# Kernel tuning notes

Measured on AMD Instinct MI355X. Metric: run time of the kernel, lower is better.

## Reference

```python
import jax, jax.numpy as jnp
import numpy as np

ZC, ZS = 32, 16
NS = [16384, 4096, 1024, 256, 64]  # mesh node counts per level
K_CH = 6
DEG = 12

def _key(i):
    return jax.random.fold_in(jax.random.key(0), i)

def setup_inputs():
    d = {}
    d["x"] = jax.random.normal(_key(0), (2, 16, NS[0], 3), jnp.float32)
    enc_dims = [(6, 16), (16, 16), (16, 16), (16, 32)]
    dec_dims = [(32, 16), (16, 16), (16, 16), (16, 3)]
    i = 1
    for p, dims in (("enc", enc_dims), ("decc", dec_dims), ("decs", dec_dims)):
        for l, (fi, fo) in enumerate(dims):
            d[p + "_W" + str(l)] = 0.1 * jax.random.normal(_key(i), (K_CH, fi, fo), jnp.float32); i += 1
            if p == "enc" or l < 3:  # last decoder convs have bias=None
                d[p + "_b" + str(l)] = jnp.zeros((fo,), jnp.float32)
    nfz = NS[4] * 32  # _n_features_before_z
    d["mu_W"] = 0.1 * jax.random.normal(_key(i), (ZC + ZS, nfz), jnp.float32); i += 1
    d["mu_b"] = jnp.zeros((ZC + ZS,), jnp.float32)
    d["linc_W"] = 0.1 * jax.random.normal(_key(i), (nfz, ZC), jnp.float32); i += 1
    d["linc_b"] = jnp.zeros((nfz,), jnp.float32)
    d["lins_W"] = 0.1 * jax.random.normal(_key(i), (nfz, ZC + 2 * ZS), jnp.float32); i += 1
    d["lins_b"] = jnp.zeros((nfz,), jnp.float32)
    for l in range(4):
        d["ei" + str(l)] = jax.random.randint(_key(i), (2, DEG * NS[l]), 0, NS[l], jnp.int32); i += 1
    d["ei4"] = jax.random.randint(_key(i), (2, DEG * NS[0]), 0, NS[0], jnp.int32); i += 1
    for l in range(4):
        d["ds_i" + str(l)] = jax.random.randint(_key(i), (NS[l + 1], 3), 0, NS[l], jnp.int32); i += 1
        d["ds_w" + str(l)] = jax.random.uniform(_key(i), (NS[l + 1], 3), jnp.float32); i += 1
        d["us_i" + str(l)] = jax.random.randint(_key(i), (NS[l], 3), 0, NS[l + 1], jnp.int32); i += 1
        d["us_w" + str(l)] = jax.random.uniform(_key(i), (NS[l], 3), jnp.float32); i += 1
    return d

def _norm(ei, n):
    # ChebConv_Coma.norm: D^-1/2 A D^-1/2 edge weights (unit edge weights)
    row, col = ei[0], ei[1]
    deg = jnp.zeros((n,), jnp.float32).at[row].add(1.0)
    dis = jnp.where(deg > 0, 1.0 / jnp.sqrt(jnp.maximum(deg, 1.0)), 0.0)
    return dis[row] * dis[col]

def _prop(x, ei, w, n):
    # sparse matvec: out[:, dst] += w_e * x[:, src]   (x: [B, n, F])
    msg = x[:, ei[0], :] * w[None, :, None]
    return jnp.zeros((x.shape[0], n, x.shape[2]), x.dtype).at[:, ei[1], :].add(msg)

def _cheb(x, ei, w, Wk, b, n):
    # Chebyshev recurrence: T0=x, T1=Lx, Tk=2L T_{k-1} - T_{k-2}
    out = jnp.einsum('bnf,fg->bng', x, Wk[0])
    Tx0 = x
    Tx1 = _prop(x, ei, w, n)
    out = out + jnp.einsum('bnf,fg->bng', Tx1, Wk[1])
    for k in range(2, Wk.shape[0]):
        Tx2 = 2.0 * _prop(Tx1, ei, w, n) - Tx0
        out = out + jnp.einsum('bnf,fg->bng', Tx2, Wk[k])
        Tx0, Tx1 = Tx1, Tx2
    return out if b is None else out + b

def _pool(x, idx, w):
    # sparse pooling matrix, 3 nnz/row: out[:, i] = sum_k w[i,k] * x[:, idx[i,k]]
    return jnp.einsum('bnkf,nk->bnf', x[:, idx, :], w)

def _phase(x):
    # PhaseTensor: doubles last dim with cos/sin phase modulation over time axis 1
    T = x.shape[1]
    th = 2.0 * jnp.pi * jnp.arange(T, dtype=x.dtype) / T
    shp = (1, T) + (1,) * (x.ndim - 2)
    return jnp.concatenate([x * jnp.cos(th).reshape(shp), x * jnp.sin(th).reshape(shp)], axis=-1)

def _model(FL, IL):
    (x, eW0, eb0, eW1, eb1, eW2, eb2, eW3, eb3,
     cW0, cb0, cW1, cb1, cW2, cb2, cW3,
     sW0, sb0, sW1, sb1, sW2, sb2, sW3,
     mu_W, mu_b, linc_W, linc_b, lins_W, lins_b,
     ds_w0, ds_w1, ds_w2, ds_w3, us_w0, us_w1, us_w2, us_w3) = FL
    (ei0, ei1, ei2, ei3, ei4,
     ds_i0, ds_i1, ds_i2, ds_i3, us_i0, us_i1, us_i2, us_i3) = IL
    eis = [ei0, ei1, ei2, ei3, ei4]
    lvl_n = [NS[0], NS[1], NS[2], NS[3], NS[0]]
    nrm = [_norm(eis[l], lvl_n[l]) for l in range(5)]
    B, T, N0, F0 = x.shape
    # phase_input: [B,T,N,3] -> [B,T,N,6]; fold time into batch for the conv stack
    h = _phase(x).reshape(B * T, N0, 2 * F0)
    encW = [(eW0, eb0), (eW1, eb1), (eW2, eb2), (eW3, eb3)]
    dsl = [(ds_i0, ds_w0), (ds_i1, ds_w1), (ds_i2, ds_w2), (ds_i3, ds_w3)]
    usl = [(us_i0, us_w0), (us_i1, us_w1), (us_i2, us_w2), (us_i3, us_w3)]
    for l in range(4):
        h = jax.nn.relu(_cheb(h, eis[l], nrm[l], encW[l][0], encW[l][1], NS[l]))
        h = _pool(h, dsl[l][0], dsl[l][1])
    h = h.reshape(B, T, -1)  # [B, T, N4*32]
    mu = jnp.einsum('btf,zf->btz', h, mu_W) + mu_b
    # faithful to torch code: per-t cat along dim 0 (time-major) then reshape(-1, T, z)
    mu_c = jnp.mean(jnp.swapaxes(mu[..., :ZC], 0, 1).reshape(B, T, ZC), axis=1)
    mu_s = jnp.mean(jnp.swapaxes(mu[..., ZC:], 0, 1).reshape(B, T, ZS), axis=1)

    def dec(z, Ws, bs, lW, lb, relu_first):
        y = z @ lW.T + lb
        if relu_first:
            y = jax.nn.relu(y)
        y = y.reshape(y.shape[0], NS[4], Ws[0].shape[1])  # [*, N4, 32]
        for i in range(3):  # n_layers - 1 upsample+conv+relu
            lvl = 3 - i
            y = _pool(y, usl[lvl][0], usl[lvl][1])
            y = jax.nn.relu(_cheb(y, eis[lvl], nrm[lvl], Ws[i], bs[i], NS[lvl]))
        y = _pool(y, usl[0][0], usl[0][1])
        return _cheb(y, eis[4], nrm[4], Ws[3], None, NS[0])  # final conv, no bias/relu

    s_avg = dec(mu_c, [cW0, cW1, cW2, cW3], [cb0, cb1, cb2], linc_W, linc_b, False)
    # decoder_s, vectorized over timeframes by folding T into batch
    zs_ph = _phase(jnp.broadcast_to(mu_s[:, None, :], (B, T, ZS)))  # [B,T,2*ZS]
    zc_rep = jnp.broadcast_to(mu_c[:, None, :], (B, T, ZC))
    zin = jnp.concatenate([zc_rep, zs_ph], axis=-1).reshape(B * T, ZC + 2 * ZS)
    ds_t = dec(zin, [sW0, sW1, sW2, sW3], [sb0, sb1, sb2], lins_W, lins_b, True).reshape(B, T, N0, 3)
    s_t = s_avg[:, None] + ds_t
    return mu_c, mu_s, s_avg, s_t

def reference(x, enc_W0, enc_b0, enc_W1, enc_b1, enc_W2, enc_b2, enc_W3, enc_b3, decc_W0, decc_b0, decc_W1, decc_b1, decc_W2, decc_b2, decc_W3, decs_W0, decs_b0, decs_W1, decs_b1, decs_W2, decs_b2, decs_W3, mu_W, mu_b, linc_W, linc_b, lins_W, lins_b, ds_w0, ds_w1, ds_w2, ds_w3, us_w0, us_w1, us_w2, us_w3, ei0, ei1, ei2, ei3, ei4, ds_i0, ds_i1, ds_i2, ds_i3, us_i0, us_i1, us_i2, us_i3):
    FL = (x, enc_W0, enc_b0, enc_W1, enc_b1, enc_W2, enc_b2, enc_W3, enc_b3,
          decc_W0, decc_b0, decc_W1, decc_b1, decc_W2, decc_b2, decc_W3,
          decs_W0, decs_b0, decs_W1, decs_b1, decs_W2, decs_b2, decs_W3,
          mu_W, mu_b, linc_W, linc_b, lins_W, lins_b,
          ds_w0, ds_w1, ds_w2, ds_w3, us_w0, us_w1, us_w2, us_w3)
    IL = (ei0, ei1, ei2, ei3, ei4, ds_i0, ds_i1, ds_i2, ds_i3, us_i0, us_i1, us_i2, us_i3)
    return _model(FL, IL)
```

## Files before the change

### kernel.cpp

```cpp
#include <hip/hip_runtime.h>
#include <cstdint>
#include <cstddef>

#define TPB 256

typedef float f32x4 __attribute__((ext_vector_type(4)));
typedef float f32x2 __attribute__((ext_vector_type(2)));
typedef int   i32x4 __attribute__((ext_vector_type(4)));

static inline int cdiv(long long a, int b){ return (int)((a + (long long)b - 1) / b); }

#define NTOT 38144
#define ETOT 457728
#define CTOT 762880
#define RPTOT 38149


template<int W>
__device__ __forceinline__ void vload(const float* __restrict__ p, float* r){
  if constexpr (W == 8){ vload<4>(p, r); vload<4>(p+4, r+4); }
  else if constexpr (W == 4){ f32x4 v = *reinterpret_cast<const f32x4*>(p); r[0]=v.x;r[1]=v.y;r[2]=v.z;r[3]=v.w; }
  else { f32x2 v = *reinterpret_cast<const f32x2*>(p); r[0]=v.x;r[1]=v.y; }
}
template<int W>
__device__ __forceinline__ void vstore(float* __restrict__ p, const float* r){
  if constexpr (W == 8){ vstore<4>(p, r); vstore<4>(p+4, r+4); }
  else if constexpr (W == 4){ f32x4 v; v.x=r[0];v.y=r[1];v.z=r[2];v.w=r[3]; *reinterpret_cast<f32x4*>(p) = v; }
  else { f32x2 v; v.x=r[0];v.y=r[1]; *reinterpret_cast<f32x2*>(p) = v; }
}

template<int F>
__device__ __forceinline__ void loadrow(const float* __restrict__ p, float* r){
  #pragma unroll
  for (int q = 0; q < F/4; ++q) vload<4>(p + 4*q, r + 4*q);
}
template<int F>
__device__ __forceinline__ void storerow(float* __restrict__ p, const float* r){
  #pragma unroll
  for (int q = 0; q < F/4; ++q) vstore<4>(p + 4*q, r + 4*q);
}


__device__ __forceinline__ bool lvl_edge(int t, const int* e0,const int* e1,const int* e2,const int* e3,const int* e4,
                                         const int*& ei, int& E, int& noff, int& rpoff, int& rel){
  if (t < 196608){ ei=e0; E=196608; noff=0;     rpoff=0;     rel=t;        return true; }
  if (t < 245760){ ei=e1; E=49152;  noff=16384; rpoff=16385; rel=t-196608; return true; }
  if (t < 258048){ ei=e2; E=12288;  noff=20480; rpoff=20482; rel=t-245760; return true; }
  if (t < 261120){ ei=e3; E=3072;   noff=21504; rpoff=21507; rel=t-258048; return true; }
  if (t < 457728){ ei=e4; E=196608; noff=21760; rpoff=21764; rel=t-261120; return true; }
  return false;
}

__global__ void k_degs_all(const int* e0,const int* e1,const int* e2,const int* e3,const int* e4,
                           int* __restrict__ rowdeg, int* __restrict__ dstdeg){
  int t = blockIdx.x*blockDim.x + threadIdx.x;
  const int* ei; int E, noff, rpoff, rel;
  if (!lvl_edge(t, e0,e1,e2,e3,e4, ei,E,noff,rpoff,rel)) return;
  atomicAdd(&rowdeg[noff + ei[rel]], 1);
  atomicAdd(&dstdeg[noff + ei[E + rel]], 1);
}

__global__ void k_dis_all(const int* __restrict__ rowdeg, float* __restrict__ dis){
  int t = blockIdx.x*blockDim.x + threadIdx.x;
  if (t >= NTOT) return;
  int d = rowdeg[t];
  dis[t] = d > 0 ? rsqrtf((float)d) : 0.f;
}

__global__ void k_scan5(const int* __restrict__ dstdeg, int* __restrict__ rp, int* __restrict__ cursor){
  const int NnA[5]  = {16384,4096,1024,256,16384};
  const int NOFF[5] = {0,16384,20480,21504,21760};
  const int COFF[5] = {0,327680,409600,430080,435200};
  __shared__ int part[257];
  int l = blockIdx.x;
  int N = NnA[l];
  const int* cnt = dstdeg + NOFF[l];
  int* rpl = rp + NOFF[l] + l;
  int* cul = cursor + NOFF[l] + l;
  int tid = threadIdx.x;
  int chunk = (N + 255) / 256;
  int lo = tid*chunk; if (lo > N) lo = N;
  int hi = lo + chunk; if (hi > N) hi = N;
  int s = 0;
  for (int i = lo; i < hi; ++i) s += (cnt[i] + 7) & ~7;
  part[tid+1] = s;
  if (tid == 0) part[0] = COFF[l];
  __syncthreads();
  if (tid == 0){ for (int i = 1; i <= 256; ++i) part[i] += part[i-1]; }
  __syncthreads();
  int run = part[tid];
  for (int i = lo; i < hi; ++i){ rpl[i] = run; cul[i] = run; run += (cnt[i] + 7) & ~7; }
  if (tid == 0) rpl[N] = part[256];
}

__global__ void k_fill_all(const int* e0,const int* e1,const int* e2,const int* e3,const int* e4,
                           const float* __restrict__ dis, int* __restrict__ cursor,
                           int* __restrict__ srcs, float* __restrict__ w){
  int t = blockIdx.x*blockDim.x + threadIdx.x;
  const int* ei; int E, noff, rpoff, rel;
  if (!lvl_edge(t, e0,e1,e2,e3,e4, ei,E,noff,rpoff,rel)) return;
  int src = ei[rel], dst = ei[E + rel];
  int pos = atomicAdd(&cursor[rpoff + dst], 1);
  srcs[pos] = src;
  w[pos] = dis[noff + src] * dis[noff + dst];
}

__global__ void k_pad_all(const int* __restrict__ dstdeg, const int* __restrict__ rp,
                          int* __restrict__ srcs, float* __restrict__ w){
  int t = blockIdx.x*blockDim.x + threadIdx.x;
  if (t >= NTOT) return;
  int rpoff, n;
  if      (t < 16384){ rpoff = 0;     n = t; }
  else if (t < 20480){ rpoff = 16385; n = t - 16384; }
  else if (t < 21504){ rpoff = 20482; n = t - 20480; }
  else if (t < 21760){ rpoff = 21507; n = t - 21504; }
  else               { rpoff = 21764; n = t - 21760; }
  int j0 = rp[rpoff + n];
  int j1 = rp[rpoff + n + 1];
  int cnt = dstdeg[t];
  int sfill = cnt > 0 ? srcs[j0] : 0;
  for (int j = j0 + cnt; j < j1; ++j){ srcs[j] = sfill; w[j] = 0.f; }
}


template<int FPL, int FinPad>
__device__ __forceinline__ void gather8(const float* __restrict__ gb,
                                        const int* __restrict__ srcs, const float* __restrict__ w,
                                        int j0, int j1, int sub, float* acc){
  #pragma unroll
  for (int q = 0; q < FPL; ++q) acc[q] = 0.f;
  for (int j = j0; j < j1; j += 8){
    i32x4 sa = *reinterpret_cast<const i32x4*>(srcs + j);
    i32x4 sb = *reinterpret_cast<const i32x4*>(srcs + j + 4);
    f32x4 wa = *reinterpret_cast<const f32x4*>(w + j);
    f32x4 wb = *reinterpret_cast<const f32x4*>(w + j + 4);
    float v0[FPL], v1[FPL], v2[FPL], v3[FPL], v4[FPL], v5[FPL], v6[FPL], v7[FPL];
    vload<FPL>(gb + (size_t)sa.x*FinPad + sub*FPL, v0);
    vload<FPL>(gb + (size_t)sa.y*FinPad + sub*FPL, v1);
    vload<FPL>(gb + (size_t)sa.z*FinPad + sub*FPL, v2);
    vload<FPL>(gb + (size_t)sa.w*FinPad + sub*FPL, v3);
    vload<FPL>(gb + (size_t)sb.x*FinPad + sub*FPL, v4);
    vload<FPL>(gb + (size_t)sb.y*FinPad + sub*FPL, v5);
    vload<FPL>(gb + (size_t)sb.z*FinPad + sub*FPL, v6);
    vload<FPL>(gb + (size_t)sb.w*FinPad + sub*FPL, v7);
    #pragma unroll
    for (int q = 0; q < FPL; ++q){
      acc[q] = fmaf(wa.x, v0[q], acc[q]);
      acc[q] = fmaf(wa.y, v1[q], acc[q]);
      acc[q] = fmaf(wa.z, v2[q], acc[q]);
      acc[q] = fmaf(wa.w, v3[q], acc[q]);
      acc[q] = fmaf(wb.x, v4[q], acc[q]);
      acc[q] = fmaf(wb.y, v5[q], acc[q]);
      acc[q] = fmaf(wb.z, v6[q], acc[q]);
      acc[q] = fmaf(wb.w, v7[q], acc[q]);
    }
  }
}

template<int FinPad, int FinReal, int Fout>
__device__ __forceinline__ void gemm_acc(const float* ts, const float* __restrict__ Wk,
                                         int sub, int lanebase, float* o){
  constexpr int FPL = FinPad/4;
  float tv[FinPad];
  #pragma unroll
  for (int s = 0; s < 4; ++s)
    #pragma unroll
    for (int q = 0; q < FPL; ++q)
      tv[s*FPL+q] = __shfl(ts[q], lanebase + s, 64);
  if constexpr (Fout % 4 == 0){
    constexpr int OPL = Fout/4;
    #pragma unroll
    for (int fi = 0; fi < FinReal; ++fi)
      #pragma unroll
      for (int q = 0; q < OPL; ++q)
        o[q] = fmaf(tv[fi], Wk[fi*Fout + sub*OPL + q], o[q]);
  } else {
    if (sub < Fout){
      #pragma unroll
      for (int fi = 0; fi < FinReal; ++fi)
        o[0] = fmaf(tv[fi], Wk[fi*Fout + sub], o[0]);
    }
  }
}

__device__ __forceinline__ long long swz_i(int G){
  int bid = blockIdx.x, nb = gridDim.x;
  if (G == 32 && (nb & 31) == 0){
    int bpg = nb >> 5;
    int xcd = bid & 7, j = bid >> 3;
    int gi = j / bpg, nc = j - gi*bpg;
    bid = ((gi << 3) | xcd) * bpg + nc;
  }
  return (long long)bid * blockDim.x + threadIdx.x;
}

template<int FinPad, int PRE>
__device__ __forceinline__ void pre_row(const float* __restrict__ psrc, const int* __restrict__ pidx,
                                        const float* __restrict__ pw, int n, int g, int Nin, int sub,
                                        float* r){
  constexpr int FPL = FinPad/4;
  if constexpr (PRE == 1){
    int t = g & 15;
    float th = 6.283185307179586f * (float)t / 16.0f;
    float sn, cs; sincosf(th, &sn, &cs);
    const float* xr = psrc + ((size_t)g*16384 + n)*3;
    #pragma unroll
    for (int q = 0; q < FPL; ++q){
      int c = sub*FPL + q;
      float v = 0.f;
      if (c < 6) v = xr[c % 3] * (c < 3 ? cs : sn);
      r[q] = v;
    }
  } else {
    int i0 = pidx[n*3+0], i1 = pidx[n*3+1], i2 = pidx[n*3+2];
    float w0 = pw[n*3+0], w1 = pw[n*3+1], w2 = pw[n*3+2];
    const float* bsrc = psrc + (size_t)g*Nin*FinPad + sub*FPL;
    float a[FPL], b[FPL], c[FPL];
    vload<FPL>(bsrc + (size_t)i0*FinPad, a);
    vload<FPL>(bsrc + (size_t)i1*FinPad, b);
    vload<FPL>(bsrc + (size_t)i2*FinPad, c);
    #pragma unroll
    for (int q = 0; q < FPL; ++q) r[q] = fmaf(w0, a[q], fmaf(w1, b[q], w2*c[q]));
  }
}


template<int FinPad, int PRE>
__global__ void k_pre_f(const float* __restrict__ psrc, const int* __restrict__ pidx,
                        const float* __restrict__ pw, float* __restrict__ bufX,
                        int G, int logN, int Nin){
  constexpr int FPL = FinPad/4;
  long long i4 = swz_i(G);
  if (i4 >= ((long long)G << logN)*4) return;
  int sub = (int)(i4 & 3);
  long long i = i4 >> 2;
  int N = 1 << logN;
  int n = (int)(i & (N-1));
  int g = (int)(i >> logN);
  float r[FPL];
  pre_row<FinPad,PRE>(psrc, pidx, pw, n, g, Nin, sub, r);
  vstore<FPL>(bufX + (size_t)i*FinPad + sub*FPL, r);
}

template<int FinPad, int FinReal, int Fout>
__global__ void k_first_f(const int* __restrict__ rp, const int* __restrict__ srcs, const float* __restrict__ w,
                          const float* __restrict__ bufX, float* __restrict__ bufT1, float* __restrict__ out,
                          const float* __restrict__ W6, const float* __restrict__ bias,
                          int G, int logN){
  constexpr int FPL = FinPad/4;
  constexpr int OPL = (Fout % 4 == 0) ? Fout/4 : 1;
  long long i4 = swz_i(G);
  if (i4 >= ((long long)G << logN)*4) return;
  int sub = (int)(i4 & 3);
  long long i = i4 >> 2;
  int N = 1 << logN;
  int n = (int)(i & (N-1));
  int lanebase = ((int)threadIdx.x & 63) & ~3;
  const float* gb = bufX + (size_t)(i - n)*FinPad;
  float t0[FPL]; vload<FPL>(bufX + (size_t)i*FinPad + sub*FPL, t0);
  float t1[FPL];
  gather8<FPL,FinPad>(gb, srcs, w, rp[n], rp[n+1], sub, t1);
  vstore<FPL>(bufT1 + (size_t)i*FinPad + sub*FPL, t1);
  float o[OPL];
  if constexpr (Fout % 4 == 0){
    #pragma unroll
    for (int q = 0; q < OPL; ++q) o[q] = bias ? bias[sub*OPL + q] : 0.f;
  } else {
    o[0] = (bias && sub < Fout) ? bias[sub] : 0.f;
  }
  gemm_acc<FinPad,FinReal,Fout>(t0, W6, sub, lanebase, o);
  gemm_acc<FinPad,FinReal,Fout>(t1, W6 + (size_t)FinReal*Fout, sub, lanebase, o);
  if constexpr (Fout % 4 == 0) vstore<OPL>(out + (size_t)i*Fout + sub*OPL, o);
  else if (sub < Fout) out[(size_t)i*Fout + sub] = o[0];
}

template<int FinPad, int FinReal, int Fout>
__global__ void k_step_f(const int* __restrict__ rp, const int* __restrict__ srcs, const float* __restrict__ w,
                         const float* __restrict__ Tm1, float* __restrict__ P, float* __restrict__ out,
                         const float* __restrict__ Wk, const float* __restrict__ savg,
                         int G, int logN, int relu, int last){
  constexpr int FPL = FinPad/4;
  constexpr int OPL = (Fout % 4 == 0) ? Fout/4 : 1;
  long long i4 = swz_i(G);
  if (i4 >= ((long long)G << logN)*4) return;
  int sub = (int)(i4 & 3);
  long long i = i4 >> 2;
  int N = 1 << logN;
  int n = (int)(i & (N-1));
  int lanebase = ((int)threadIdx.x & 63) & ~3;
  const float* gb = Tm1 + (size_t)(i - n)*FinPad;
  float tk[FPL];
  gather8<FPL,FinPad>(gb, srcs, w, rp[n], rp[n+1], sub, tk);
  float tm2[FPL]; vload<FPL>(P + (size_t)i*FinPad + sub*FPL, tm2);
  #pragma unroll
  for (int q = 0; q < FPL; ++q) tk[q] = 2.f*tk[q] - tm2[q];
  if (!last) vstore<FPL>(P + (size_t)i*FinPad + sub*FPL, tk);
  float o[OPL];
  if constexpr (Fout % 4 == 0) vload<OPL>(out + (size_t)i*Fout + sub*OPL, o);
  else { o[0] = (sub < Fout) ? out[(size_t)i*Fout + sub] : 0.f; }
  gemm_acc<FinPad,FinReal,Fout>(tk, Wk, sub, lanebase, o);
  if constexpr (Fout % 4 == 0){
    if (last && relu){
      #pragma unroll
      for (int q = 0; q < OPL; ++q) o[q] = fmaxf(o[q], 0.f);
    }
    vstore<OPL>(out + (size_t)i*Fout + sub*OPL, o);
  } else {
    if (sub < Fout){
      float v = o[0];
      if (last && relu) v = fmaxf(v, 0.f);
      if (last && savg){
        int g = (int)(i >> logN);
        int b = g >> 4;
        v += savg[((size_t)b*N + n)*3 + sub];
      }
      out[(size_t)i*Fout + sub] = v;
    }
  }
}


template<int F>
__global__ void k_pool_t(const float* __restrict__ X, const int* __restrict__ idx,
                         const float* __restrict__ w, float* __restrict__ out,
                         int G, int Nin, int Nout){
  long long i = (long long)blockIdx.x*blockDim.x + threadIdx.x;
  if (i >= (long long)G*Nout) return;
  int n = (int)(i % Nout), g = (int)(i / Nout);
  int i0 = idx[n*3+0], i1 = idx[n*3+1], i2 = idx[n*3+2];
  float w0 = w[n*3+0], w1 = w[n*3+1], w2 = w[n*3+2];
  const float* b = X + (size_t)g*Nin*F;
  float r0[F], r1[F], r2[F], o[F];
  loadrow<F>(b + (size_t)i0*F, r0);
  loadrow<F>(b + (size_t)i1*F, r1);
  loadrow<F>(b + (size_t)i2*F, r2);
  #pragma unroll
  for (int f = 0; f < F; ++f)
    o[f] = fmaf(w0, r0[f], fmaf(w1, r1[f], w2 * r2[f]));
  storerow<F>(out + ((size_t)g*Nout + n)*F, o);
}

__global__ void k_mu(const float* __restrict__ h, const float* __restrict__ W,
                     const float* __restrict__ b, float* __restrict__ mu){
  int wid = (blockIdx.x*blockDim.x + threadIdx.x) >> 6;
  int lane = threadIdx.x & 63;
  if (wid >= 32*48) return;
  int z = wid % 48, g = wid / 48;
  const float* hr = h + (size_t)g*2048;
  const float* wr = W + (size_t)z*2048;
  float acc = 0.f;
  for (int f = lane; f < 2048; f += 64) acc = fmaf(hr[f], wr[f], acc);
  for (int o = 32; o > 0; o >>= 1) acc += __shfl_down(acc, o, 64);
  if (lane == 0) mu[wid] = acc + b[z];
}

__global__ void k_mucs(const float* __restrict__ mu, float* __restrict__ muc,
                       float* __restrict__ mus, float* __restrict__ out){
  int i = blockIdx.x*blockDim.x + threadIdx.x;
  if (i >= 96) return;
  int z = i % 48, bp = i / 48;
  float acc = 0.f;
  for (int b = 0; b < 2; ++b)
    for (int t = 8*bp; t < 8*bp + 8; ++t)
      acc += mu[(b*16 + t)*48 + z];
  acc *= (1.f/16.f);
  if (z < 32){ muc[bp*32 + z] = acc; out[bp*32 + z] = acc; }
  else       { mus[bp*16 + (z-32)] = acc; out[64 + bp*16 + (z-32)] = acc; }
}

__global__ void k_zin(const float* __restrict__ muc, const float* __restrict__ mus,
                      float* __restrict__ zin){
  int i = blockIdx.x*blockDim.x + threadIdx.x;
  if (i >= 32*64) return;
  int c = i % 64, g = i / 64;
  int b = g / 16, t = g % 16;
  float v;
  if (c < 32){
    v = muc[b*32 + c];
  } else {
    float th = 6.283185307179586f * (float)t / 16.0f;
    int k = c - 32;
    int kk = (k < 16) ? k : (k - 16);
    float m = mus[b*16 + kk];
    v = (k < 16) ? m * cosf(th) : m * sinf(th);
  }
  zin[i] = v;
}

__global__ void k_lin(const float* __restrict__ z, const float* __restrict__ W,
                      const float* __restrict__ b, float* __restrict__ y,
                      int G, int Z, int relu){
  int i = blockIdx.x*blockDim.x + threadIdx.x;
  if (i >= G*2048) return;
  int f = i % 2048, g = i / 2048;
  const float* zr = z + (size_t)g*Z;
  const float* wr = W + (size_t)f*Z;
  float acc = b[f];
  for (int k = 0; k < Z; ++k) acc = fmaf(zr[k], wr[k], acc);
  if (relu) acc = fmaxf(acc, 0.f);
  y[i] = acc;
}


struct LvlArgs {
  const int* rp; const int* srcs; const float* w;
  const float* psrc; const int* pidx; const float* pw;
  float* bufX; float* bufT1; float* out;
  const float* W6; const float* bias; const float* savg;
  int G; int logN; int Nin; int relu;
};

template<int FinPad, int FinReal, int Fout, int PRE>
static void run_level(hipStream_t s, const LvlArgs& a){
  long long GN4 = ((long long)a.G << a.logN) * 4;
  int grid = cdiv(GN4, 256);
  k_pre_f<FinPad,PRE><<<grid,256,0,s>>>(a.psrc, a.pidx, a.pw, a.bufX, a.G, a.logN, a.Nin);
  k_first_f<FinPad,FinReal,Fout><<<grid,256,0,s>>>(a.rp, a.srcs, a.w, a.bufX, a.bufT1, a.out,
                                                   a.W6, a.bias, a.G, a.logN);
  float* Ab = a.bufT1; float* Bb = a.bufX;
  for (int k = 2; k <= 5; ++k){
    int last = (k == 5) ? 1 : 0;
    k_step_f<FinPad,FinReal,Fout><<<grid,256,0,s>>>(a.rp, a.srcs, a.w, Ab, Bb, a.out,
                                                    a.W6 + (size_t)k*FinReal*Fout,
                                                    last ? a.savg : nullptr,
                                                    a.G, a.logN, a.relu, last);
    float* t = Ab; Ab = Bb; Bb = t;
  }
}

extern "C" void kernel_launch(void* const* d_in, const int* in_sizes, int n_in,
                              void* d_out, int out_size, void* d_ws, size_t ws_size,
                              hipStream_t stream){
  const float* x = (const float*)d_in[0];
  const float* encW[4] = {(const float*)d_in[1],(const float*)d_in[3],(const float*)d_in[5],(const float*)d_in[7]};
  const float* encB[4] = {(const float*)d_in[2],(const float*)d_in[4],(const float*)d_in[6],(const float*)d_in[8]};
  const float* ccW[4]  = {(const float*)d_in[9],(const float*)d_in[11],(const float*)d_in[13],(const float*)d_in[15]};
  const float* ccB[3]  = {(const float*)d_in[10],(const float*)d_in[12],(const float*)d_in[14]};
  const float* csW[4]  = {(const float*)d_in[16],(const float*)d_in[18],(const float*)d_in[20],(const float*)d_in[22]};
  const float* csB[3]  = {(const float*)d_in[17],(const float*)d_in[19],(const float*)d_in[21]};
  const float* muW  = (const float*)d_in[23]; const float* muB  = (const float*)d_in[24];
  const float* lincW = (const float*)d_in[25]; const float* lincB = (const float*)d_in[26];
  const float* linsW = (const float*)d_in[27]; const float* linsB = (const float*)d_in[28];
  const int* ei[5] = {(const int*)d_in[29],(const int*)d_in[30],(const int*)d_in[31],
                      (const int*)d_in[32],(const int*)d_in[33]};
  const int* ds_i[4]; const float* ds_w[4]; const int* us_i[4]; const float* us_w[4];
  for (int l = 0; l < 4; ++l){
    ds_i[l] = (const int*)d_in[34 + 4*l]; ds_w[l] = (const float*)d_in[35 + 4*l];
    us_i[l] = (const int*)d_in[36 + 4*l]; us_w[l] = (const float*)d_in[37 + 4*l];
  }

  float* ws = (float*)d_ws;
  const size_t BIG = 8388608;
  float* B0 = ws + 0*BIG;
  float* B1 = ws + 1*BIG;
  float* B2 = ws + 2*BIG;
  float* B3 = ws + 3*BIG;
  size_t off = 4*BIG;

  int*   rp_all     = (int*)(ws + off); off += RPTOT;
  int*   cursor_all = (int*)(ws + off); off += RPTOT;
  off = (off + 3) & ~(size_t)3;
  int*   srcs_all   = (int*)(ws + off); off += CTOT;
  float* w_all      =        ws + off;  off += CTOT;
  int*   rowdeg     = (int*)(ws + off); off += NTOT;
  int*   dstdeg     = (int*)(ws + off); off += NTOT;
  float* dis        =        ws + off;  off += NTOT;
  float* hmu        =        ws + off;  off += (size_t)32*2048;
  float* mu         =        ws + off;  off += (size_t)32*48;
  float* muc        =        ws + off;  off += 64;
  float* mus        =        ws + off;  off += 32;
  float* zin        =        ws + off;  off += (size_t)32*64;

  float* outp = (float*)d_out;
  float* out_savg = outp + 96;
  float* out_st   = outp + 96 + 98304;

  hipMemsetAsync(rowdeg, 0, 2*(size_t)NTOT*sizeof(int), stream);
  k_degs_all<<<cdiv(ETOT,TPB),TPB,0,stream>>>(ei[0],ei[1],ei[2],ei[3],ei[4], rowdeg, dstdeg);
  k_dis_all<<<cdiv(NTOT,TPB),TPB,0,stream>>>(rowdeg, dis);
  k_scan5<<<5,256,0,stream>>>(dstdeg, rp_all, cursor_all);
  k_fill_all<<<cdiv(ETOT,TPB),TPB,0,stream>>>(ei[0],ei[1],ei[2],ei[3],ei[4], dis, cursor_all, srcs_all, w_all);
  k_pad_all<<<cdiv(NTOT,TPB),TPB,0,stream>>>(dstdeg, rp_all, srcs_all, w_all);

  const int RPOFF[5] = {0,16385,20482,21507,21764};
  const int* RP[5];
  for (int l = 0; l < 5; ++l) RP[l] = rp_all + RPOFF[l];

  run_level<8,6,16,1>(stream, {RP[0],srcs_all,w_all, x,nullptr,nullptr,
                               B0,B1,B2, encW[0],encB[0],nullptr, 32,14,0,1});
  run_level<16,16,16,0>(stream, {RP[1],srcs_all,w_all, B2,ds_i[0],ds_w[0],
                                 B0,B1,B3, encW[1],encB[1],nullptr, 32,12,16384,1});
  run_level<16,16,16,0>(stream, {RP[2],srcs_all,w_all, B3,ds_i[1],ds_w[1],
                                 B0,B1,B2, encW[2],encB[2],nullptr, 32,10,4096,1});
  run_level<16,16,32,0>(stream, {RP[3],srcs_all,w_all, B2,ds_i[2],ds_w[2],
                                 B0,B1,B3, encW[3],encB[3],nullptr, 32,8,1024,1});
  k_pool_t<32><<<cdiv((long long)32*64,TPB),TPB,0,stream>>>(B3, ds_i[3], ds_w[3], hmu, 32, 256, 64);

  k_mu<<<cdiv((long long)32*48*64,TPB),TPB,0,stream>>>(hmu, muW, muB, mu);
  k_mucs<<<1,128,0,stream>>>(mu, muc, mus, outp);

  k_lin<<<cdiv((long long)2*2048,TPB),TPB,0,stream>>>(muc, lincW, lincB, B2, 2, 32, 0);
  run_level<32,32,16,0>(stream, {RP[3],srcs_all,w_all, B2,us_i[3],us_w[3],
                                 B0,B1,B3, ccW[0],ccB[0],nullptr, 2,8,64,1});
  run_level<16,16,16,0>(stream, {RP[2],srcs_all,w_all, B3,us_i[2],us_w[2],
                                 B0,B1,B2, ccW[1],ccB[1],nullptr, 2,10,256,1});
  run_level<16,16,16,0>(stream, {RP[1],srcs_all,w_all, B2,us_i[1],us_w[1],
                                 B0,B1,B3, ccW[2],ccB[2],nullptr, 2,12,1024,1});
  run_level<16,16,3,0>(stream, {RP[4],srcs_all,w_all, B3,us_i[0],us_w[0],
                                B0,B1,out_savg, ccW[3],nullptr,nullptr, 2,14,4096,0});

  k_zin<<<cdiv(32*64,TPB),TPB,0,stream>>>(muc, mus, zin);
  k_lin<<<cdiv((long long)32*2048,TPB),TPB,0,stream>>>(zin, linsW, linsB, B2, 32, 64, 1);
  run_level<32,32,16,0>(stream, {RP[3],srcs_all,w_all, B2,us_i[3],us_w[3],
                                 B0,B1,B3, csW[0],csB[0],nullptr, 32,8,64,1});
  run_level<16,16,16,0>(stream, {RP[2],srcs_all,w_all, B3,us_i[2],us_w[2],
                                 B0,B1,B2, csW[1],csB[1],nullptr, 32,10,256,1});
  run_level<16,16,16,0>(stream, {RP[1],srcs_all,w_all, B2,us_i[1],us_w[1],
                                 B0,B1,B3, csW[2],csB[2],nullptr, 32,12,1024,1});
  run_level<16,16,3,0>(stream, {RP[4],srcs_all,w_all, B3,us_i[0],us_w[0],
                                B0,B1,out_st, csW[3],nullptr,out_savg, 32,14,4096,0});

  (void)in_sizes; (void)n_in; (void)out_size; (void)ws_size;
}
```

Before: 1.326 ms.

## Interleave four graphs per node row for batched Chebyshev convolutions

Adds a transposed layout for the 32-graph paths: each node row now holds the features of four graphs side by side, and the grid is split into eight graph-groups with one group per block-index residue mod 8. Each gathered neighbour index then serves four graphs with one contiguous fetch, which cuts index and weight loads and improves the coalescing of the sparse gather. The pooling, mu projection and lins linear kernels are rewritten to produce or consume this layout. The 2-graph content decoder keeps the old layout without the XCD swizzle. The cost is more complex indexing and wider per-row footprints.

```diff
diff --git a/kernel.cpp b/kernel.cpp
--- a/kernel.cpp
+++ b/kernel.cpp
@@ -123,6 +123,192 @@
 }
 
 
+template<int FinPad>
+__device__ __forceinline__ void tmap(int N, int& gb, int& n, int& gs, int& sub, int& laneoff){
+  constexpr int LPR = FinPad/4;
+  gb = blockIdx.x & 7;
+  int I = (blockIdx.x >> 3)*256 + threadIdx.x;
+  n = I / FinPad;
+  int u = I - n*FinPad;
+  gs = u / LPR;
+  sub = u - gs*LPR;
+  laneoff = gs*FinPad + sub*4;
+}
+
+template<int FinPad>
+__device__ __forceinline__ void gather8_t(const float* __restrict__ base,
+                                          const int* __restrict__ srcs, const float* __restrict__ w,
+                                          int j0, int j1, int laneoff, float* acc){
+  constexpr int RS = 4*FinPad;
+  #pragma unroll
+  for (int q = 0; q < 4; ++q) acc[q] = 0.f;
+  for (int j = j0; j < j1; j += 8){
+    i32x4 sa = *reinterpret_cast<const i32x4*>(srcs + j);
+    i32x4 sb = *reinterpret_cast<const i32x4*>(srcs + j + 4);
+    f32x4 wa = *reinterpret_cast<const f32x4*>(w + j);
+    f32x4 wb = *reinterpret_cast<const f32x4*>(w + j + 4);
+    float v0[4], v1[4], v2[4], v3[4], v4[4], v5[4], v6[4], v7[4];
+    vload<4>(base + (size_t)sa.x*RS + laneoff, v0);
+    vload<4>(base + (size_t)sa.y*RS + laneoff, v1);
+    vload<4>(base + (size_t)sa.z*RS + laneoff, v2);
+    vload<4>(base + (size_t)sa.w*RS + laneoff, v3);
+    vload<4>(base + (size_t)sb.x*RS + laneoff, v4);
+    vload<4>(base + (size_t)sb.y*RS + laneoff, v5);
+    vload<4>(base + (size_t)sb.z*RS + laneoff, v6);
+    vload<4>(base + (size_t)sb.w*RS + laneoff, v7);
+    #pragma unroll
+    for (int q = 0; q < 4; ++q){
+      acc[q] = fmaf(wa.x, v0[q], acc[q]);
+      acc[q] = fmaf(wa.y, v1[q], acc[q]);
+      acc[q] = fmaf(wa.z, v2[q], acc[q]);
+      acc[q] = fmaf(wa.w, v3[q], acc[q]);
+      acc[q] = fmaf(wb.x, v4[q], acc[q]);
+      acc[q] = fmaf(wb.y, v5[q], acc[q]);
+      acc[q] = fmaf(wb.z, v6[q], acc[q]);
+      acc[q] = fmaf(wb.w, v7[q], acc[q]);
+    }
+  }
+}
+
+template<int FinPad, int FinReal, int Fout>
+__device__ __forceinline__ void gemm_t(const float* ts, const float* __restrict__ Wk,
+                                       int sub, float* o){
+  constexpr int LPR = FinPad/4;
+  int lane = (int)threadIdx.x & 63;
+  int lanebase = lane & ~(LPR-1);
+  float tv[FinPad];
+  #pragma unroll
+  for (int s = 0; s < LPR; ++s)
+    #pragma unroll
+    for (int q = 0; q < 4; ++q)
+      tv[s*4+q] = __shfl(ts[q], lanebase + s, 64);
+  if constexpr (Fout % 4 == 0){
+    constexpr int OPL = Fout/LPR;
+    #pragma unroll
+    for (int fi = 0; fi < FinReal; ++fi)
+      #pragma unroll
+      for (int q = 0; q < OPL; ++q)
+        o[q] = fmaf(tv[fi], Wk[fi*Fout + sub*OPL + q], o[q]);
+  } else {
+    if (sub < Fout){
+      #pragma unroll
+      for (int fi = 0; fi < FinReal; ++fi)
+        o[0] = fmaf(tv[fi], Wk[fi*Fout + sub], o[0]);
+    }
+  }
+}
+
+template<int FinPad, int PRE>
+__global__ void k_pre_t(const float* __restrict__ psrc, const int* __restrict__ pidx,
+                        const float* __restrict__ pw, float* __restrict__ bufX,
+                        int N, int Nin){
+  int gb, n, gs, sub, laneoff;
+  tmap<FinPad>(N, gb, n, gs, sub, laneoff);
+  constexpr int RS = 4*FinPad;
+  float r[4];
+  if constexpr (PRE == 1){
+    int g = (gb<<2) | gs;
+    int t = g & 15;
+    float th = 6.283185307179586f * (float)t / 16.0f;
+    float sn, cs; sincosf(th, &sn, &cs);
+    const float* xr = psrc + ((size_t)g*16384 + n)*3;
+    #pragma unroll
+    for (int q = 0; q < 4; ++q){
+      int f = sub*4 + q;
+      float v = 0.f;
+      if (f < 6) v = xr[f % 3] * (f < 3 ? cs : sn);
+      r[q] = v;
+    }
+  } else {
+    int i0 = pidx[n*3+0], i1 = pidx[n*3+1], i2 = pidx[n*3+2];
+    float w0 = pw[n*3+0], w1 = pw[n*3+1], w2 = pw[n*3+2];
+    const float* pb = psrc + (size_t)gb*Nin*RS + laneoff;
+    float a[4], b[4], c[4];
+    vload<4>(pb + (size_t)i0*RS, a);
+    vload<4>(pb + (size_t)i1*RS, b);
+    vload<4>(pb + (size_t)i2*RS, c);
+    #pragma unroll
+    for (int q = 0; q < 4; ++q) r[q] = fmaf(w0, a[q], fmaf(w1, b[q], w2*c[q]));
+  }
+  vstore<4>(bufX + (size_t)gb*N*RS + (size_t)n*RS + laneoff, r);
+}
+
+template<int FinPad, int FinReal, int Fout>
+__global__ void k_first_t(const int* __restrict__ rp, const int* __restrict__ srcs, const float* __restrict__ w,
+                          const float* __restrict__ bufX, float* __restrict__ bufT1, float* __restrict__ out,
+                          const float* __restrict__ W6, const float* __restrict__ bias, int N){
+  constexpr int LPR = FinPad/4;
+  constexpr int OPL = (Fout % 4 == 0) ? Fout/LPR : 1;
+  constexpr int RS = 4*FinPad;
+  int gb, n, gs, sub, laneoff;
+  tmap<FinPad>(N, gb, n, gs, sub, laneoff);
+  const float* gbase = bufX + (size_t)gb*N*RS;
+  float t0[4]; vload<4>(gbase + (size_t)n*RS + laneoff, t0);
+  float t1[4];
+  gather8_t<FinPad>(gbase, srcs, w, rp[n], rp[n+1], laneoff, t1);
+  vstore<4>(bufT1 + (size_t)gb*N*RS + (size_t)n*RS + laneoff, t1);
+  float o[OPL];
+  if constexpr (Fout % 4 == 0){
+    #pragma unroll
+    for (int q = 0; q < OPL; ++q) o[q] = bias ? bias[sub*OPL + q] : 0.f;
+  } else {
+    o[0] = (bias && sub < Fout) ? bias[sub] : 0.f;
+  }
+  gemm_t<FinPad,FinReal,Fout>(t0, W6, sub, o);
+  gemm_t<FinPad,FinReal,Fout>(t1, W6 + (size_t)FinReal*Fout, sub, o);
+  if constexpr (Fout % 4 == 0){
+    vstore<OPL>(out + ((size_t)(gb*N + n)*4 + gs)*Fout + sub*OPL, o);
+  } else {
+    if (sub < Fout){
+      int g = (gb<<2)|gs;
+      out[((size_t)g*N + n)*3 + sub] = o[0];
+    }
+  }
+}
+
+template<int FinPad, int FinReal, int Fout>
+__global__ void k_step_t(const int* __restrict__ rp, const int* __restrict__ srcs, const float* __restrict__ w,
+                         const float* __restrict__ Tm1, float* __restrict__ P, float* __restrict__ out,
+                         const float* __restrict__ Wk, const float* __restrict__ savg,
+                         int N, int relu, int last){
+  constexpr int LPR = FinPad/4;
+  constexpr int OPL = (Fout % 4 == 0) ? Fout/LPR : 1;
+  constexpr int RS = 4*FinPad;
+  int gb, n, gs, sub, laneoff;
+  tmap<FinPad>(N, gb, n, gs, sub, laneoff);
+  const float* gbase = Tm1 + (size_t)gb*N*RS;
+  float tk[4];
+  gather8_t<FinPad>(gbase, srcs, w, rp[n], rp[n+1], laneoff, tk);
+  float tm2[4]; vload<4>(P + (size_t)gb*N*RS + (size_t)n*RS + laneoff, tm2);
+  #pragma unroll
+  for (int q = 0; q < 4; ++q) tk[q] = 2.f*tk[q] - tm2[q];
+  if (!last) vstore<4>(P + (size_t)gb*N*RS + (size_t)n*RS + laneoff, tk);
+  float o[OPL];
+  if constexpr (Fout % 4 == 0){
+    vload<OPL>(out + ((size_t)(gb*N + n)*4 + gs)*Fout + sub*OPL, o);
+  } else {
+    o[0] = 0.f;
+    if (sub < Fout) o[0] = out[((size_t)((gb<<2)|gs)*N + n)*3 + sub];
+  }
+  gemm_t<FinPad,FinReal,Fout>(tk, Wk, sub, o);
+  if constexpr (Fout % 4 == 0){
+    if (last && relu){
+      #pragma unroll
+      for (int q = 0; q < OPL; ++q) o[q] = fmaxf(o[q], 0.f);
+    }
+    vstore<OPL>(out + ((size_t)(gb*N + n)*4 + gs)*Fout + sub*OPL, o);
+  } else {
+    if (sub < Fout){
+      float v = o[0];
+      if (last && relu) v = fmaxf(v, 0.f);
+      int g = (gb<<2)|gs;
+      if (last && savg) v += savg[((size_t)(g>>4)*N + n)*3 + sub];
+      out[((size_t)g*N + n)*3 + sub] = v;
+    }
+  }
+}
+
+
 template<int FPL, int FinPad>
 __device__ __forceinline__ void gather8(const float* __restrict__ gb,
                                         const int* __restrict__ srcs, const float* __restrict__ w,
@@ -183,54 +369,28 @@
   }
 }
 
-__device__ __forceinline__ long long swz_i(int G){
-  int bid = blockIdx.x, nb = gridDim.x;
-  if (G == 32 && (nb & 31) == 0){
-    int bpg = nb >> 5;
-    int xcd = bid & 7, j = bid >> 3;
-    int gi = j / bpg, nc = j - gi*bpg;
-    bid = ((gi << 3) | xcd) * bpg + nc;
-  }
-  return (long long)bid * blockDim.x + threadIdx.x;
-}
-
-template<int FinPad, int PRE>
-__device__ __forceinline__ void pre_row(const float* __restrict__ psrc, const int* __restrict__ pidx,
-                                        const float* __restrict__ pw, int n, int g, int Nin, int sub,
-                                        float* r){
+template<int FinPad>
+__device__ __forceinline__ void pool_row(const float* __restrict__ psrc, const int* __restrict__ pidx,
+                                         const float* __restrict__ pw, int n, int g, int Nin, int sub,
+                                         float* r){
   constexpr int FPL = FinPad/4;
-  if constexpr (PRE == 1){
-    int t = g & 15;
-    float th = 6.283185307179586f * (float)t / 16.0f;
-    float sn, cs; sincosf(th, &sn, &cs);
-    const float* xr = psrc + ((size_t)g*16384 + n)*3;
-    #pragma unroll
-    for (int q = 0; q < FPL; ++q){
-      int c = sub*FPL + q;
-      float v = 0.f;
-      if (c < 6) v = xr[c % 3] * (c < 3 ? cs : sn);
-      r[q] = v;
-    }
-  } else {
-    int i0 = pidx[n*3+0], i1 = pidx[n*3+1], i2 = pidx[n*3+2];
-    float w0 = pw[n*3+0], w1 = pw[n*3+1], w2 = pw[n*3+2];
-    const float* bsrc = psrc + (size_t)g*Nin*FinPad + sub*FPL;
-    float a[FPL], b[FPL], c[FPL];
-    vload<FPL>(bsrc + (size_t)i0*FinPad, a);
-    vload<FPL>(bsrc + (size_t)i1*FinPad, b);
-    vload<FPL>(bsrc + (size_t)i2*FinPad, c);
-    #pragma unroll
-    for (int q = 0; q < FPL; ++q) r[q] = fmaf(w0, a[q], fmaf(w1, b[q], w2*c[q]));
-  }
-}
-
-
-template<int FinPad, int PRE>
+  int i0 = pidx[n*3+0], i1 = pidx[n*3+1], i2 = pidx[n*3+2];
+  float w0 = pw[n*3+0], w1 = pw[n*3+1], w2 = pw[n*3+2];
+  const float* bsrc = psrc + (size_t)g*Nin*FinPad + sub*FPL;
+  float a[FPL], b[FPL], c[FPL];
+  vload<FPL>(bsrc + (size_t)i0*FinPad, a);
+  vload<FPL>(bsrc + (size_t)i1*FinPad, b);
+  vload<FPL>(bsrc + (size_t)i2*FinPad, c);
+  #pragma unroll
+  for (int q = 0; q < FPL; ++q) r[q] = fmaf(w0, a[q], fmaf(w1, b[q], w2*c[q]));
+}
+
+template<int FinPad>
 __global__ void k_pre_f(const float* __restrict__ psrc, const int* __restrict__ pidx,
                         const float* __restrict__ pw, float* __restrict__ bufX,
                         int G, int logN, int Nin){
   constexpr int FPL = FinPad/4;
-  long long i4 = swz_i(G);
+  long long i4 = (long long)blockIdx.x*blockDim.x + threadIdx.x;
   if (i4 >= ((long long)G << logN)*4) return;
   int sub = (int)(i4 & 3);
   long long i = i4 >> 2;
@@ -238,7 +398,7 @@
   int n = (int)(i & (N-1));
   int g = (int)(i >> logN);
   float r[FPL];
-  pre_row<FinPad,PRE>(psrc, pidx, pw, n, g, Nin, sub, r);
+  pool_row<FinPad>(psrc, pidx, pw, n, g, Nin, sub, r);
   vstore<FPL>(bufX + (size_t)i*FinPad + sub*FPL, r);
 }
 
@@ -249,7 +409,7 @@
                           int G, int logN){
   constexpr int FPL = FinPad/4;
   constexpr int OPL = (Fout % 4 == 0) ? Fout/4 : 1;
-  long long i4 = swz_i(G);
+  long long i4 = (long long)blockIdx.x*blockDim.x + threadIdx.x;
   if (i4 >= ((long long)G << logN)*4) return;
   int sub = (int)(i4 & 3);
   long long i = i4 >> 2;
@@ -281,7 +441,7 @@
                          int G, int logN, int relu, int last){
   constexpr int FPL = FinPad/4;
   constexpr int OPL = (Fout % 4 == 0) ? Fout/4 : 1;
-  long long i4 = swz_i(G);
+  long long i4 = (long long)blockIdx.x*blockDim.x + threadIdx.x;
   if (i4 >= ((long long)G << logN)*4) return;
   int sub = (int)(i4 & 3);
   long long i = i4 >> 2;
@@ -311,8 +471,7 @@
       if (last && relu) v = fmaxf(v, 0.f);
       if (last && savg){
         int g = (int)(i >> logN);
-        int b = g >> 4;
-        v += savg[((size_t)b*N + n)*3 + sub];
+        v += savg[((size_t)(g>>4)*N + n)*3 + sub];
       }
       out[(size_t)i*Fout + sub] = v;
     }
@@ -320,36 +479,17 @@
 }
 
 
-template<int F>
-__global__ void k_pool_t(const float* __restrict__ X, const int* __restrict__ idx,
-                         const float* __restrict__ w, float* __restrict__ out,
-                         int G, int Nin, int Nout){
-  long long i = (long long)blockIdx.x*blockDim.x + threadIdx.x;
-  if (i >= (long long)G*Nout) return;
-  int n = (int)(i % Nout), g = (int)(i / Nout);
-  int i0 = idx[n*3+0], i1 = idx[n*3+1], i2 = idx[n*3+2];
-  float w0 = w[n*3+0], w1 = w[n*3+1], w2 = w[n*3+2];
-  const float* b = X + (size_t)g*Nin*F;
-  float r0[F], r1[F], r2[F], o[F];
-  loadrow<F>(b + (size_t)i0*F, r0);
-  loadrow<F>(b + (size_t)i1*F, r1);
-  loadrow<F>(b + (size_t)i2*F, r2);
-  #pragma unroll
-  for (int f = 0; f < F; ++f)
-    o[f] = fmaf(w0, r0[f], fmaf(w1, r1[f], w2 * r2[f]));
-  storerow<F>(out + ((size_t)g*Nout + n)*F, o);
-}
-
-__global__ void k_mu(const float* __restrict__ h, const float* __restrict__ W,
-                     const float* __restrict__ b, float* __restrict__ mu){
+__global__ void k_mu_t(const float* __restrict__ h_t, const float* __restrict__ W,
+                       const float* __restrict__ b, float* __restrict__ mu){
   int wid = (blockIdx.x*blockDim.x + threadIdx.x) >> 6;
   int lane = threadIdx.x & 63;
   if (wid >= 32*48) return;
   int z = wid % 48, g = wid / 48;
-  const float* hr = h + (size_t)g*2048;
   const float* wr = W + (size_t)z*2048;
+  const float* hb = h_t + (size_t)(g>>2)*64*128 + (g&3)*32;
   float acc = 0.f;
-  for (int f = lane; f < 2048; f += 64) acc = fmaf(hr[f], wr[f], acc);
+  for (int f2 = lane; f2 < 2048; f2 += 64)
+    acc = fmaf(hb[(size_t)(f2>>5)*128 + (f2&31)], wr[f2], acc);
   for (int o = 32; o > 0; o >>= 1) acc += __shfl_down(acc, o, 64);
   if (lane == 0) mu[wid] = acc + b[z];
 }
@@ -401,6 +541,20 @@
   y[i] = acc;
 }
 
+__global__ void k_lin_t(const float* __restrict__ z, const float* __restrict__ W,
+                        const float* __restrict__ b, float* __restrict__ y_t,
+                        int Z, int relu){
+  int i = blockIdx.x*blockDim.x + threadIdx.x;
+  if (i >= 32*2048) return;
+  int f2 = i % 2048, g = i / 2048;
+  const float* zr = z + (size_t)g*Z;
+  const float* wr = W + (size_t)f2*Z;
+  float acc = b[f2];
+  for (int k = 0; k < Z; ++k) acc = fmaf(zr[k], wr[k], acc);
+  if (relu) acc = fmaxf(acc, 0.f);
+  y_t[(size_t)(g>>2)*64*128 + (size_t)(f2>>5)*128 + (g&3)*32 + (f2&31)] = acc;
+}
+
 
 struct LvlArgs {
   const int* rp; const int* srcs; const float* w;
@@ -411,10 +565,28 @@
 };
 
 template<int FinPad, int FinReal, int Fout, int PRE>
-static void run_level(hipStream_t s, const LvlArgs& a){
+static void run_level_t(hipStream_t s, const LvlArgs& a){
+  int N = 1 << a.logN;
+  int grid = 8 * (N*FinPad/256);
+  k_pre_t<FinPad,PRE><<<grid,256,0,s>>>(a.psrc, a.pidx, a.pw, a.bufX, N, a.Nin);
+  k_first_t<FinPad,FinReal,Fout><<<grid,256,0,s>>>(a.rp, a.srcs, a.w, a.bufX, a.bufT1, a.out,
+                                                   a.W6, a.bias, N);
+  float* Ab = a.bufT1; float* Bb = a.bufX;
+  for (int k = 2; k <= 5; ++k){
+    int last = (k == 5) ? 1 : 0;
+    k_step_t<FinPad,FinReal,Fout><<<grid,256,0,s>>>(a.rp, a.srcs, a.w, Ab, Bb, a.out,
+                                                    a.W6 + (size_t)k*FinReal*Fout,
+                                                    last ? a.savg : nullptr,
+                                                    N, a.relu, last);
+    float* t = Ab; Ab = Bb; Bb = t;
+  }
+}
+
+template<int FinPad, int FinReal, int Fout>
+static void run_level_f(hipStream_t s, const LvlArgs& a){
   long long GN4 = ((long long)a.G << a.logN) * 4;
   int grid = cdiv(GN4, 256);
-  k_pre_f<FinPad,PRE><<<grid,256,0,s>>>(a.psrc, a.pidx, a.pw, a.bufX, a.G, a.logN, a.Nin);
+  k_pre_f<FinPad><<<grid,256,0,s>>>(a.psrc, a.pidx, a.pw, a.bufX, a.G, a.logN, a.Nin);
   k_first_f<FinPad,FinReal,Fout><<<grid,256,0,s>>>(a.rp, a.srcs, a.w, a.bufX, a.bufT1, a.out,
                                                    a.W6, a.bias, a.G, a.logN);
   float* Ab = a.bufT1; float* Bb = a.bufX;
@@ -486,39 +658,42 @@
   const int* RP[5];
   for (int l = 0; l < 5; ++l) RP[l] = rp_all + RPOFF[l];
 
-  run_level<8,6,16,1>(stream, {RP[0],srcs_all,w_all, x,nullptr,nullptr,
-                               B0,B1,B2, encW[0],encB[0],nullptr, 32,14,0,1});
-  run_level<16,16,16,0>(stream, {RP[1],srcs_all,w_all, B2,ds_i[0],ds_w[0],
-                                 B0,B1,B3, encW[1],encB[1],nullptr, 32,12,16384,1});
-  run_level<16,16,16,0>(stream, {RP[2],srcs_all,w_all, B3,ds_i[1],ds_w[1],
-                                 B0,B1,B2, encW[2],encB[2],nullptr, 32,10,4096,1});
-  run_level<16,16,32,0>(stream, {RP[3],srcs_all,w_all, B2,ds_i[2],ds_w[2],
-                                 B0,B1,B3, encW[3],encB[3],nullptr, 32,8,1024,1});
-  k_pool_t<32><<<cdiv((long long)32*64,TPB),TPB,0,stream>>>(B3, ds_i[3], ds_w[3], hmu, 32, 256, 64);
-
-  k_mu<<<cdiv((long long)32*48*64,TPB),TPB,0,stream>>>(hmu, muW, muB, mu);
+  run_level_t<8,6,16,1>(stream, {RP[0],srcs_all,w_all, x,nullptr,nullptr,
+                                 B0,B1,B2, encW[0],encB[0],nullptr, 32,14,0,1});
+  run_level_t<16,16,16,0>(stream, {RP[1],srcs_all,w_all, B2,ds_i[0],ds_w[0],
+                                   B0,B1,B3, encW[1],encB[1],nullptr, 32,12,16384,1});
+  run_level_t<16,16,16,0>(stream, {RP[2],srcs_all,w_all, B3,ds_i[1],ds_w[1],
+                                   B0,B1,B2, encW[2],encB[2],nullptr, 32,10,4096,1});
+  run_level_t<16,16,32,0>(stream, {RP[3],srcs_all,w_all, B2,ds_i[2],ds_w[2],
+                                   B0,B1,B3, encW[3],encB[3],nullptr, 32,8,1024,1});
+  {
+    int grid = 8 * (64*32/256);
+    k_pre_t<32,0><<<grid,256,0,stream>>>(B3, ds_i[3], ds_w[3], hmu, 64, 256);
+  }
+
+  k_mu_t<<<cdiv((long long)32*48*64,TPB),TPB,0,stream>>>(hmu, muW, muB, mu);
   k_mucs<<<1,128,0,stream>>>(mu, muc, mus, outp);
 
   k_lin<<<cdiv((long long)2*2048,TPB),TPB,0,stream>>>(muc, lincW, lincB, B2, 2, 32, 0);
-  run_level<32,32,16,0>(stream, {RP[3],srcs_all,w_all, B2,us_i[3],us_w[3],
+  run_level_f<32,32,16>(stream, {RP[3],srcs_all,w_all, B2,us_i[3],us_w[3],
                                  B0,B1,B3, ccW[0],ccB[0],nullptr, 2,8,64,1});
-  run_level<16,16,16,0>(stream, {RP[2],srcs_all,w_all, B3,us_i[2],us_w[2],
+  run_level_f<16,16,16>(stream, {RP[2],srcs_all,w_all, B3,us_i[2],us_w[2],
                                  B0,B1,B2, ccW[1],ccB[1],nullptr, 2,10,256,1});
-  run_level<16,16,16,0>(stream, {RP[1],srcs_all,w_all, B2,us_i[1],us_w[1],
+  run_level_f<16,16,16>(stream, {RP[1],srcs_all,w_all, B2,us_i[1],us_w[1],
                                  B0,B1,B3, ccW[2],ccB[2],nullptr, 2,12,1024,1});
-  run_level<16,16,3,0>(stream, {RP[4],srcs_all,w_all, B3,us_i[0],us_w[0],
+  run_level_f<16,16,3>(stream, {RP[4],srcs_all,w_all, B3,us_i[0],us_w[0],
                                 B0,B1,out_savg, ccW[3],nullptr,nullptr, 2,14,4096,0});
 
   k_zin<<<cdiv(32*64,TPB),TPB,0,stream>>>(muc, mus, zin);
-  k_lin<<<cdiv((long long)32*2048,TPB),TPB,0,stream>>>(zin, linsW, linsB, B2, 32, 64, 1);
-  run_level<32,32,16,0>(stream, {RP[3],srcs_all,w_all, B2,us_i[3],us_w[3],
-                                 B0,B1,B3, csW[0],csB[0],nullptr, 32,8,64,1});
-  run_level<16,16,16,0>(stream, {RP[2],srcs_all,w_all, B3,us_i[2],us_w[2],
-                                 B0,B1,B2, csW[1],csB[1],nullptr, 32,10,256,1});
-  run_level<16,16,16,0>(stream, {RP[1],srcs_all,w_all, B2,us_i[1],us_w[1],
-                                 B0,B1,B3, csW[2],csB[2],nullptr, 32,12,1024,1});
-  run_level<16,16,3,0>(stream, {RP[4],srcs_all,w_all, B3,us_i[0],us_w[0],
-                                B0,B1,out_st, csW[3],nullptr,out_savg, 32,14,4096,0});
+  k_lin_t<<<cdiv((long long)32*2048,TPB),TPB,0,stream>>>(zin, linsW, linsB, B2, 64, 1);
+  run_level_t<32,32,16,0>(stream, {RP[3],srcs_all,w_all, B2,us_i[3],us_w[3],
+                                   B0,B1,B3, csW[0],csB[0],nullptr, 32,8,64,1});
+  run_level_t<16,16,16,0>(stream, {RP[2],srcs_all,w_all, B3,us_i[2],us_w[2],
+                                   B0,B1,B2, csW[1],csB[1],nullptr, 32,10,256,1});
+  run_level_t<16,16,16,0>(stream, {RP[1],srcs_all,w_all, B2,us_i[1],us_w[1],
+                                   B0,B1,B3, csW[2],csB[2],nullptr, 32,12,1024,1});
+  run_level_t<16,16,3,0>(stream, {RP[4],srcs_all,w_all, B3,us_i[0],us_w[0],
+                                  B0,B1,out_st, csW[3],nullptr,out_savg, 32,14,4096,0});
 
   (void)in_sizes; (void)n_in; (void)out_size; (void)ws_size;
 }
```

New measurement: 1.103 ms. 16.8% less time.
